# Kernel optimization log

Hardware: AMD Instinct MI355X
Metric: run time of the kernel (lower is better)

Reference implementation:

```python
import jax, jax.numpy as jnp
import numpy as np
from jax import lax

K_NEIGH = 10


def setup_inputs() -> dict:
    key = jax.random.key(0)
    k1, k2, k3, k4, k5 = jax.random.split(key, 5)
    bs, C, T = 8, 256, 2048
    x = jax.random.normal(k1, (bs, C, T), dtype=jnp.float32)
    num_frms = jax.random.randint(k2, (bs,), 0, 2048)
    # Conv1d(in=C, out=C, kernel=3, pad=1): weight [out, in, k], bias [out]
    conv_w = jax.random.normal(k3, (C, C, 3), dtype=jnp.float32) * (1.0 / np.sqrt(3 * C))
    conv_b = jnp.zeros((C,), dtype=jnp.float32)
    # Linear(2*C -> C): weight [out, 2*in], bias [out]
    mlp_w = jax.random.normal(k4, (C, 2 * C), dtype=jnp.float32) * (1.0 / np.sqrt(2 * C))
    mlp_b = jax.random.normal(k5, (C,), dtype=jnp.float32) * 0.01
    return {"x": x, "num_frms": num_frms, "conv_w": conv_w, "conv_b": conv_b,
            "mlp_w": mlp_w, "mlp_b": mlp_b}


def _knn_idx(x, k):
    # x: [bs, C, T]; dif[b,i,j] = ||x[b,:,i] - x[b,:,j]||^2 via norm expansion
    sq = jnp.sum(x * x, axis=1)                      # [bs, T]
    gram = jnp.einsum('bci,bcj->bij', x, x)          # [bs, T, T]
    dif = sq[:, :, None] + sq[:, None, :] - 2.0 * gram
    _, idx = lax.top_k(-dif, k)                      # k smallest distances
    return idx                                       # [bs, T, k]


def reference(x, num_frms, conv_w, conv_b, mlp_w, mlp_b):
    bs, C, T = x.shape
    Cout = conv_w.shape[0]
    # temporal conv branch (kernel 3, stride 1, pad 1)
    c_out = lax.conv_general_dilated(
        x, conv_w, window_strides=(1,), padding=((1, 1),),
        dimension_numbers=('NCH', 'OIH', 'NCH')) + conv_b[None, :, None]
    # graph branch ('par': knn on x)
    idx = _knn_idx(x, K_NEIGH)                                   # [bs, T, k]
    idx_flat = (idx + jnp.arange(bs)[:, None, None] * T).reshape(-1, K_NEIGH)
    feat = x.transpose(0, 2, 1).reshape(bs * T, C)               # [N, C]
    feat_neigh = feat[idx_flat]                                  # [N, k, C]
    ctr = feat[:, None, :]                                       # [N, 1, C]
    cat = jnp.concatenate(
        [feat_neigh, jnp.broadcast_to(ctr, feat_neigh.shape)], axis=-1)  # [N,k,2C]
    g = jnp.einsum('nkc,oc->nko', cat, mlp_w) + mlp_b            # [N, k, Cout]
    # cosine edge weight
    num = jnp.einsum('nkc,nc->nk', feat_neigh, feat)
    den = jnp.sqrt(jnp.sum(feat_neigh * feat_neigh, axis=2)) * \
          jnp.sqrt(jnp.sum(feat * feat, axis=1))[:, None]
    w = num / den                                                # [N, k]
    g = g * w[:, :, None]
    g = jnp.max(g, axis=1)                                       # [N, Cout]
    g_out = g.reshape(bs, T, Cout).transpose(0, 2, 1)            # [bs, Cout, T]
    out = jax.nn.relu(c_out + g_out)
    # MaxPool1d(kernel=2, stride=2)
    out = out.reshape(bs, Cout, T // 2, 2).max(axis=-1)
    return out
```

## Files before the change

### kernel.cpp

```cpp
#include <hip/hip_runtime.h>
#include <hip/hip_bf16.h>
#include <cstdint>

#define T_DIM 2048
#define C_DIM 256
#define BS 8
#define NPTS (BS * T_DIM)
#define KNB 10

typedef __bf16 bf16x8 __attribute__((ext_vector_type(8)));
typedef float f32x4 __attribute__((ext_vector_type(4)));

#define AS1 __attribute__((address_space(1)))
#define AS3 __attribute__((address_space(3)))

__device__ __forceinline__ unsigned short f2bf_rn(float f) {
  unsigned u = __float_as_uint(f);
  unsigned r = (u + 0x7FFFu + ((u >> 16) & 1u)) >> 16;
  return (unsigned short)r;
}
__device__ __forceinline__ float bfbits2f(unsigned short h) {
  return __uint_as_float((unsigned)h << 16);
}
__device__ __forceinline__ __bf16 bfbits(unsigned short h) {
  return __builtin_bit_cast(__bf16, h);
}

__device__ __forceinline__ void stage_tile(const __bf16* __restrict__ src, size_t row0,
                                           int ld, int k0, __bf16* lds, int w, int l) {
  int kofs = ((l & 7) ^ (l >> 3)) * 8;
  const __bf16* g0 = src + (row0 + (size_t)(l >> 3)) * ld + k0 + kofs;
  __bf16* lbase = lds + (size_t)(w * 4) * 512;
#pragma unroll
  for (int q4 = 0; q4 < 4; ++q4) {
    __builtin_amdgcn_global_load_lds((AS1 void*)(g0 + (size_t)(w * 4 + q4) * 8 * ld),
                                     (AS3 void*)(lbase + q4 * 512), 16, 0, 0);
  }
}

__device__ __forceinline__ void stage_tile_conv(const __bf16* __restrict__ src, int m0,
                                                int k0in, const __bf16* __restrict__ zp,
                                                __bf16* lds, int w, int l) {
  int tap = k0in >> 8;
  int kshift = tap - 1;
  int k0 = k0in & 255;
  int kofs = ((l & 7) ^ (l >> 3)) * 8;
  int mb = m0 & (T_DIM - 1);
#pragma unroll
  for (int q4 = 0; q4 < 4; ++q4) {
    int q = w * 4 + q4;
    int row = q * 8 + (l >> 3);
    int t = mb + row + kshift;
    const __bf16* g = ((unsigned)t < (unsigned)T_DIM)
                          ? (src + (size_t)(m0 + row + kshift) * C_DIM + k0 + kofs)
                          : (zp + kofs);
    __builtin_amdgcn_global_load_lds((AS1 void*)g, (AS3 void*)(lds + q * 512), 16, 0, 0);
  }
}

__device__ __forceinline__ bf16x8 read_frag(const __bf16* lds, int t16, int ks, int l) {
  int row = t16 * 16 + (l & 15);
  int kb = ks * 64 + ((l >> 4) << 4);
  int byte = row * 128 + (kb ^ ((row & 7) << 4));
  return *(const bf16x8*)((const char*)lds + byte);
}

__global__ __launch_bounds__(256) void k_transpose_split(const float* __restrict__ x,
                                                         __bf16* __restrict__ Fh,
                                                         __bf16* __restrict__ Fl) {
  __shared__ float tile[32][33];
  int b = blockIdx.z;
  int t0 = blockIdx.x * 32;
  int c0 = blockIdx.y * 32;
  int tx = threadIdx.x & 31, ty = threadIdx.x >> 5;
  const float* xb = x + (size_t)b * C_DIM * T_DIM;
#pragma unroll
  for (int r = 0; r < 4; ++r) {
    int c = c0 + ty + 8 * r;
    tile[ty + 8 * r][tx] = xb[(size_t)c * T_DIM + t0 + tx];
  }
  __syncthreads();
#pragma unroll
  for (int r = 0; r < 4; ++r) {
    int t = t0 + ty + 8 * r;
    float v = tile[tx][ty + 8 * r];
    unsigned short hb = f2bf_rn(v);
    float lo = v - bfbits2f(hb);
    size_t o = ((size_t)b * T_DIM + t) * C_DIM + c0 + tx;
    Fh[o] = bfbits(hb);
    Fl[o] = bfbits(f2bf_rn(lo));
  }
}

__global__ __launch_bounds__(256) void k_sq(const __bf16* __restrict__ Fh,
                                            const __bf16* __restrict__ Fl,
                                            float* __restrict__ sq) {
  int n = blockIdx.x * 4 + (threadIdx.x >> 6);
  int lane = threadIdx.x & 63;
  ushort4 hv = ((const ushort4*)Fh)[(size_t)n * 64 + lane];
  ushort4 lv = ((const ushort4*)Fl)[(size_t)n * 64 + lane];
  float s = 0.f;
  {
    float v;
    v = bfbits2f(hv.x) + bfbits2f(lv.x); s = fmaf(v, v, s);
    v = bfbits2f(hv.y) + bfbits2f(lv.y); s = fmaf(v, v, s);
    v = bfbits2f(hv.z) + bfbits2f(lv.z); s = fmaf(v, v, s);
    v = bfbits2f(hv.w) + bfbits2f(lv.w); s = fmaf(v, v, s);
  }
#pragma unroll
  for (int d = 1; d < 64; d <<= 1) s += __shfl_xor(s, d, 64);
  if (lane == 0) sq[n] = s;
}

__global__ __launch_bounds__(256, 2) void k_gram_sym(const __bf16* __restrict__ Fh,
                                                     const __bf16* __restrict__ Fl,
                                                     float* __restrict__ gram) {
  __shared__ __align__(16) char smem[65536];
  __bf16* Ah = (__bf16*)smem;
  __bf16* Al = (__bf16*)(smem + 16384);
  __bf16* Bh = (__bf16*)(smem + 32768);
  __bf16* Bl = (__bf16*)(smem + 49152);

  int b = blockIdx.y;
  int ti = blockIdx.x;
  int by = (int)((sqrtf(8.0f * (float)ti + 1.0f) - 1.0f) * 0.5f);
  if ((by + 1) * (by + 2) / 2 <= ti) by++;
  int bx = ti - by * (by + 1) / 2;

  size_t base = (size_t)b * T_DIM;
  int m0 = by * 128, n0 = bx * 128;
  int tid = threadIdx.x, w = tid >> 6, l = tid & 63;
  int wr = w >> 1, wc = w & 1;
  f32x4 acc[4][4];
#pragma unroll
  for (int i = 0; i < 4; ++i)
#pragma unroll
    for (int j = 0; j < 4; ++j) acc[i][j] = {0.f, 0.f, 0.f, 0.f};

  for (int k0 = 0; k0 < C_DIM; k0 += 64) {
    stage_tile(Fh, base + m0, C_DIM, k0, Ah, w, l);
    stage_tile(Fl, base + m0, C_DIM, k0, Al, w, l);
    stage_tile(Fh, base + n0, C_DIM, k0, Bh, w, l);
    stage_tile(Fl, base + n0, C_DIM, k0, Bl, w, l);
    __syncthreads();
#pragma unroll
    for (int ks = 0; ks < 2; ++ks) {
      bf16x8 ah[4], bh[4], x[4];
#pragma unroll
      for (int i = 0; i < 4; ++i) ah[i] = read_frag(Ah, wr * 4 + i, ks, l);
#pragma unroll
      for (int j = 0; j < 4; ++j) bh[j] = read_frag(Bh, wc * 4 + j, ks, l);
#pragma unroll
      for (int i = 0; i < 4; ++i)
#pragma unroll
        for (int j = 0; j < 4; ++j)
          acc[i][j] = __builtin_amdgcn_mfma_f32_16x16x32_bf16(ah[i], bh[j], acc[i][j], 0, 0, 0);
#pragma unroll
      for (int i = 0; i < 4; ++i) x[i] = read_frag(Al, wr * 4 + i, ks, l);
#pragma unroll
      for (int i = 0; i < 4; ++i)
#pragma unroll
        for (int j = 0; j < 4; ++j)
          acc[i][j] = __builtin_amdgcn_mfma_f32_16x16x32_bf16(x[i], bh[j], acc[i][j], 0, 0, 0);
#pragma unroll
      for (int j = 0; j < 4; ++j) x[j] = read_frag(Bl, wc * 4 + j, ks, l);
#pragma unroll
      for (int i = 0; i < 4; ++i)
#pragma unroll
        for (int j = 0; j < 4; ++j)
          acc[i][j] = __builtin_amdgcn_mfma_f32_16x16x32_bf16(ah[i], x[j], acc[i][j], 0, 0, 0);
    }
    __syncthreads();
  }

  float* gout = gram + (size_t)b * T_DIM * T_DIM;
#pragma unroll
  for (int i = 0; i < 4; ++i) {
    int mrow = m0 + wr * 64 + i * 16 + ((l >> 4) << 2);
#pragma unroll
    for (int j = 0; j < 4; ++j) {
      int ncol = n0 + wc * 64 + j * 16 + (l & 15);
      float* cp = gout + (size_t)mrow * T_DIM + ncol;
#pragma unroll
      for (int r = 0; r < 4; ++r) cp[(size_t)r * T_DIM] = acc[i][j][r];
    }
  }

  if (bx != by) {
    float* Tbuf = (float*)smem;
#pragma unroll
    for (int h = 0; h < 2; ++h) {
      __syncthreads();
      if (wc == h) {
#pragma unroll
        for (int j = 0; j < 4; ++j) {
          int cH = j * 16 + (l & 15);
          float* dst = Tbuf + cH * 132 + wr * 64 + ((l >> 4) << 2);
#pragma unroll
          for (int i = 0; i < 4; ++i) *(f32x4*)(dst + i * 16) = acc[i][j];
        }
      }
      __syncthreads();
      int cH = tid >> 5;
      int c4 = (tid & 31) * 4;
#pragma unroll
      for (int p = 0; p < 8; ++p) {
        f32x4 v = *(const f32x4*)(Tbuf + (size_t)(p * 8 + cH) * 132 + c4);
        *(f32x4*)(gout + (size_t)(n0 + h * 64 + p * 8 + cH) * T_DIM + m0 + c4) = v;
      }
    }
  }
}

__global__ __launch_bounds__(256, 2) void k_gemm16(const __bf16* __restrict__ A,
                                                   const __bf16* __restrict__ Bm,
                                                   float* __restrict__ C, int N, int K,
                                                   int conv, const __bf16* __restrict__ zp) {
  __shared__ __bf16 As[128 * 64], Bs[128 * 64];
  int m0 = blockIdx.y * 128, n0 = blockIdx.x * 128;
  int tid = threadIdx.x, w = tid >> 6, l = tid & 63;
  int wr = w >> 1, wc = w & 1;
  f32x4 acc[4][4];
#pragma unroll
  for (int i = 0; i < 4; ++i)
#pragma unroll
    for (int j = 0; j < 4; ++j) acc[i][j] = {0.f, 0.f, 0.f, 0.f};

  for (int k0 = 0; k0 < K; k0 += 64) {
    if (conv)
      stage_tile_conv(A, m0, k0, zp, As, w, l);
    else
      stage_tile(A, (size_t)m0, C_DIM, k0, As, w, l);
    stage_tile(Bm, (size_t)n0, K, k0, Bs, w, l);
    __syncthreads();
#pragma unroll
    for (int ks = 0; ks < 2; ++ks) {
      bf16x8 af[4], bf_[4];
#pragma unroll
      for (int i = 0; i < 4; ++i) af[i] = read_frag(As, wr * 4 + i, ks, l);
#pragma unroll
      for (int j = 0; j < 4; ++j) bf_[j] = read_frag(Bs, wc * 4 + j, ks, l);
#pragma unroll
      for (int i = 0; i < 4; ++i)
#pragma unroll
        for (int j = 0; j < 4; ++j)
          acc[i][j] = __builtin_amdgcn_mfma_f32_16x16x32_bf16(af[i], bf_[j], acc[i][j], 0, 0, 0);
    }
    __syncthreads();
  }
#pragma unroll
  for (int i = 0; i < 4; ++i) {
    int mrow = m0 + wr * 64 + i * 16 + ((l >> 4) << 2);
#pragma unroll
    for (int j = 0; j < 4; ++j) {
      int ncol = n0 + wc * 64 + j * 16 + (l & 15);
      float* cp = C + (size_t)mrow * N + ncol;
#pragma unroll
      for (int r = 0; r < 4; ++r) cp[(size_t)r * N] = acc[i][j][r];
    }
  }
}

__global__ __launch_bounds__(256) void k_topk(const float* __restrict__ gram,
                                              const float* __restrict__ sq,
                                              int* __restrict__ idxo,
                                              float* __restrict__ wo) {
  int lb = blockIdx.y;
  const float* gramb = gram + (size_t)lb * T_DIM * T_DIM;
  const float* sqb = sq + (size_t)lb * T_DIM;
  int* idxb = idxo + (size_t)lb * T_DIM * KNB;
  float* wbp = wo + (size_t)lb * T_DIM * KNB;

  int row = blockIdx.x * 4 + (threadIdx.x >> 6);
  int lane = threadIdx.x & 63;
  float sqi = sqb[row];
  const float* g = gramb + (size_t)row * T_DIM;

  unsigned kh[32];
  unsigned long long a0 = ~0ull, a1 = ~0ull;
#pragma unroll
  for (int t = 0; t < 32; ++t) {
    int j = lane + 64 * t;
    float dif = sqi + sqb[j] - 2.0f * g[j];
    unsigned u = __float_as_uint(dif);
    u = (u & 0x80000000u) ? ~u : (u | 0x80000000u);
    kh[t] = u;
    unsigned long long key = ((unsigned long long)u << 32) | (unsigned)j;
    unsigned long long mx = (key > a0) ? key : a0;
    a0 = (key < a0) ? key : a0;
    a1 = (mx < a1) ? mx : a1;
  }

  unsigned long long theta = 0;
#pragma unroll
  for (int s = 0; s < KNB; ++s) {
    unsigned long long m = a0;
#pragma unroll
    for (int d = 1; d < 64; d <<= 1) {
      unsigned long long o = __shfl_xor(m, d, 64);
      m = (o < m) ? o : m;
    }
    unsigned long long bal = __ballot(a0 == m);
    int leader = (int)__builtin_ctzll(bal);
    if (lane == leader) { a0 = a1; a1 = ~0ull; }
    if (lane == 0) {
      int j = (int)(unsigned)(m & 0xffffffffull);
      unsigned su = (unsigned)(m >> 32);
      unsigned bits = (su & 0x80000000u) ? (su & 0x7fffffffu) : ~su;
      float dif = __uint_as_float(bits);
      float sqj = sqb[j];
      float num = 0.5f * (sqi + sqj - dif);
      float wv = num / (sqrtf(sqi) * sqrtf(sqj));
      idxb[row * KNB + s] = j;
      wbp[row * KNB + s] = wv;
    }
    theta = m;
  }

  unsigned thi = (unsigned)(theta >> 32);
  unsigned tlo = (unsigned)(theta & 0xffffffffull);
  int c = 0;
#pragma unroll
  for (int t = 0; t < 32; ++t) {
    unsigned j = (unsigned)(lane + 64 * t);
    c += (kh[t] < thi) || ((kh[t] == thi) && (j < tlo));
  }
#pragma unroll
  for (int d = 1; d < 64; d <<= 1) c += __shfl_xor(c, d, 64);

  if (c == 9) return;

  unsigned long long b0 = ~0ull, b1 = ~0ull, b2 = ~0ull, b3 = ~0ull, b4 = ~0ull,
                     b5 = ~0ull, b6 = ~0ull, b7 = ~0ull, b8 = ~0ull, b9 = ~0ull;
#pragma unroll
  for (int t = 0; t < 32; ++t) {
    unsigned long long key = ((unsigned long long)kh[t] << 32) | (unsigned)(lane + 64 * t);
    if (key < b9) {
      b9 = key;
      unsigned long long tt;
      if (b9 < b8) { tt = b8; b8 = b9; b9 = tt; }
      if (b8 < b7) { tt = b7; b7 = b8; b8 = tt; }
      if (b7 < b6) { tt = b6; b6 = b7; b7 = tt; }
      if (b6 < b5) { tt = b5; b5 = b6; b6 = tt; }
      if (b5 < b4) { tt = b4; b4 = b5; b5 = tt; }
      if (b4 < b3) { tt = b3; b3 = b4; b4 = tt; }
      if (b3 < b2) { tt = b2; b2 = b3; b3 = tt; }
      if (b2 < b1) { tt = b1; b1 = b2; b2 = tt; }
      if (b1 < b0) { tt = b0; b0 = b1; b1 = tt; }
    }
  }
#pragma unroll
  for (int s = 0; s < KNB; ++s) {
    unsigned long long m = b0;
#pragma unroll
    for (int d = 1; d < 64; d <<= 1) {
      unsigned long long o = __shfl_xor(m, d, 64);
      m = (o < m) ? o : m;
    }
    unsigned long long bal = __ballot(b0 == m);
    int leader = (int)__builtin_ctzll(bal);
    if (lane == leader) {
      b0 = b1; b1 = b2; b2 = b3; b3 = b4; b4 = b5;
      b5 = b6; b6 = b7; b7 = b8; b8 = b9; b9 = ~0ull;
    }
    if (lane == 0) {
      int j = (int)(unsigned)(m & 0xffffffffull);
      unsigned su = (unsigned)(m >> 32);
      unsigned bits = (su & 0x80000000u) ? (su & 0x7fffffffu) : ~su;
      float dif = __uint_as_float(bits);
      float sqj = sqb[j];
      float num = 0.5f * (sqi + sqj - dif);
      float wv = num / (sqrtf(sqi) * sqrtf(sqj));
      idxb[row * KNB + s] = j;
      wbp[row * KNB + s] = wv;
    }
  }
}

__global__ __launch_bounds__(256) void k_gfinal(const float* __restrict__ mlpout,
                                                const float* __restrict__ mlp_b,
                                                const int* __restrict__ idxo,
                                                const float* __restrict__ wo,
                                                const float* __restrict__ convb,
                                                const float* __restrict__ cb,
                                                float* __restrict__ out) {
  __shared__ float tile[32][33];
  __shared__ int sj[64][KNB];
  __shared__ float sw[64][KNB];
  int b = blockIdx.z, c0 = blockIdx.y * 32, t20 = blockIdx.x * 32;
  int tid = threadIdx.x;
  int nbase = b * T_DIM + t20 * 2;
  for (int e = tid; e < 64 * KNB; e += 256) {
    int ln = e / KNB, k = e - ln * KNB;
    sj[ln][k] = b * T_DIM + idxo[(size_t)(nbase + ln) * KNB + k];
    sw[ln][k] = wo[(size_t)(nbase + ln) * KNB + k];
  }
  __syncthreads();
  int tx = tid & 31, ty = tid >> 5;
  int c = c0 + tx;
  float bias_c = cb[c];
  float mbias = mlp_b[c];
#pragma unroll
  for (int rr = 0; rr < 4; ++rr) {
    int lt2 = ty + 8 * rr;
    float res[2];
#pragma unroll
    for (int s = 0; s < 2; ++s) {
      int ln = 2 * lt2 + s;
      int n = nbase + ln;
      float q = mlpout[(size_t)n * 512 + 256 + c] + mbias;
      float mx = -3.4e38f;
#pragma unroll
      for (int k = 0; k < KNB; ++k) {
        float v = (mlpout[(size_t)sj[ln][k] * 512 + c] + q) * sw[ln][k];
        mx = fmaxf(mx, v);
      }
      float v = convb[(size_t)n * C_DIM + c] + mx + bias_c;
      res[s] = fmaxf(v, 0.f);
    }
    tile[lt2][tx] = fmaxf(res[0], res[1]);
  }
  __syncthreads();
#pragma unroll
  for (int rr = 0; rr < 4; ++rr) {
    int cc = c0 + ty + 8 * rr;
    out[((size_t)b * C_DIM + cc) * (T_DIM / 2) + t20 + tx] = tile[tx][ty + 8 * rr];
  }
}

__global__ void k_repack(const float* __restrict__ cw, const float* __restrict__ mw,
                         __bf16* __restrict__ wk3, __bf16* __restrict__ mlpB,
                         __bf16* __restrict__ zp) {
  int i = blockIdx.x * 256 + threadIdx.x;
  if (i < 3 * C_DIM * C_DIM) {
    int o = i / 768;
    int rem = i - o * 768;
    int tap = rem >> 8;
    int ii = rem & 255;
    wk3[i] = bfbits(f2bf_rn(cw[(size_t)o * 768 + ii * 3 + tap]));
  } else {
    int m = i - 3 * C_DIM * C_DIM;
    if (m < 512 * 256) {
      int r = m >> 8;
      int col = m & 255;
      mlpB[m] = bfbits(f2bf_rn(mw[(size_t)(r & 255) * 512 + ((r >> 8) << 8) + col]));
    }
  }
  if (blockIdx.x == 0 && threadIdx.x < 128) zp[threadIdx.x] = bfbits(0);
}

extern "C" void kernel_launch(void* const* d_in, const int* in_sizes, int n_in,
                              void* d_out, int out_size, void* d_ws, size_t ws_size,
                              hipStream_t stream) {
  const float* x = (const float*)d_in[0];
  const float* conv_w = (const float*)d_in[2];
  const float* conv_b = (const float*)d_in[3];
  const float* mlp_w = (const float*)d_in[4];
  const float* mlp_b = (const float*)d_in[5];
  float* out = (float*)d_out;

  char* ws = (char*)d_ws;
  size_t off = 0;
  auto alloc = [&](size_t bytes) -> void* {
    void* p = ws + off;
    off += (bytes + 255) & ~(size_t)255;
    return p;
  };
  float* gram = (float*)alloc((size_t)BS * T_DIM * T_DIM * 4);
  __bf16* Fh = (__bf16*)alloc((size_t)NPTS * C_DIM * 2);
  __bf16* Fl = (__bf16*)alloc((size_t)NPTS * C_DIM * 2);
  float* convout = (float*)alloc((size_t)NPTS * C_DIM * 4);
  float* mlpout = (float*)alloc((size_t)NPTS * 512 * 4);
  float* sq = (float*)alloc((size_t)NPTS * 4);
  int* idxb = (int*)alloc((size_t)NPTS * KNB * 4);
  float* wb = (float*)alloc((size_t)NPTS * KNB * 4);
  __bf16* wk3 = (__bf16*)alloc((size_t)3 * C_DIM * C_DIM * 2);
  __bf16* mlpB = (__bf16*)alloc((size_t)512 * 256 * 2);
  __bf16* zp = (__bf16*)alloc(512);

  k_repack<<<dim3(1280), 256, 0, stream>>>(conv_w, mlp_w, wk3, mlpB, zp);
  k_transpose_split<<<dim3(T_DIM / 32, C_DIM / 32, BS), 256, 0, stream>>>(x, Fh, Fl);
  k_sq<<<dim3(NPTS / 4), 256, 0, stream>>>(Fh, Fl, sq);

  k_gram_sym<<<dim3(136, BS), 256, 0, stream>>>(Fh, Fl, gram);
  k_topk<<<dim3(T_DIM / 4, BS), 256, 0, stream>>>(gram, sq, idxb, wb);

  k_gemm16<<<dim3(512 / 128, NPTS / 128), 256, 0, stream>>>(Fh, mlpB, mlpout, 512, 256, 0, zp);
  k_gemm16<<<dim3(256 / 128, NPTS / 128), 256, 0, stream>>>(Fh, wk3, convout, 256, 768, 1, zp);

  k_gfinal<<<dim3((T_DIM / 2) / 32, C_DIM / 32, BS), 256, 0, stream>>>(
      mlpout, mlp_b, idxb, wb, convout, conv_b, out);
}
```

Measured before the change: 189.4 us.

## Fuse Gram computation with streaming top-k and add exact fallback pass

Removes the 128 MB materialised Gram matrix by computing 64-row by 128-candidate tiles and keeping a per-lane sorted top-8 of 64-bit keys in registers, merged across lanes with shuffles. Rows whose partial lists may have dropped a true neighbour are flagged through an atomic list and recomputed exactly by a fallback kernel. The two bf16 GEMMs are also merged into one launch. The fused kernel drops symmetric reuse and runs at occupancy 1, so it does more MFMA work. It also adds a serial fallback pass whose cost depends on how many rows get flagged.

```diff
diff --git a/kernel.cpp b/kernel.cpp
--- a/kernel.cpp
+++ b/kernel.cpp
@@ -10,6 +10,7 @@
 
 typedef __bf16 bf16x8 __attribute__((ext_vector_type(8)));
 typedef float f32x4 __attribute__((ext_vector_type(4)));
+typedef unsigned long long u64;
 
 #define AS1 __attribute__((address_space(1)))
 #define AS3 __attribute__((address_space(3)))
@@ -24,6 +25,12 @@
 }
 __device__ __forceinline__ __bf16 bfbits(unsigned short h) {
   return __builtin_bit_cast(__bf16, h);
+}
+
+__device__ __forceinline__ unsigned key_hi(float sqi, float sqj, float gv) {
+  float dif = __fmaf_rn(-2.0f, gv, __fadd_rn(sqi, sqj));
+  unsigned u = __float_as_uint(dif);
+  return (u & 0x80000000u) ? ~u : (u | 0x80000000u);
 }
 
 __device__ __forceinline__ void stage_tile(const __bf16* __restrict__ src, size_t row0,
@@ -34,6 +41,18 @@
 #pragma unroll
   for (int q4 = 0; q4 < 4; ++q4) {
     __builtin_amdgcn_global_load_lds((AS1 void*)(g0 + (size_t)(w * 4 + q4) * 8 * ld),
+                                     (AS3 void*)(lbase + q4 * 512), 16, 0, 0);
+  }
+}
+
+__device__ __forceinline__ void stage_tile64(const __bf16* __restrict__ src, size_t row0,
+                                             int k0, __bf16* lds, int w, int l) {
+  int kofs = ((l & 7) ^ (l >> 3)) * 8;
+  const __bf16* g0 = src + (row0 + (size_t)(l >> 3)) * C_DIM + k0 + kofs;
+  __bf16* lbase = lds + (size_t)(w * 2) * 512;
+#pragma unroll
+  for (int q4 = 0; q4 < 2; ++q4) {
+    __builtin_amdgcn_global_load_lds((AS1 void*)(g0 + (size_t)(w * 2 + q4) * 8 * C_DIM),
                                      (AS3 void*)(lbase + q4 * 512), 16, 0, 0);
   }
 }
@@ -112,267 +131,287 @@
   if (lane == 0) sq[n] = s;
 }
 
-__global__ __launch_bounds__(256, 2) void k_gram_sym(const __bf16* __restrict__ Fh,
+
+__global__ __launch_bounds__(256, 1) void k_gramtopk(const __bf16* __restrict__ Fh,
                                                      const __bf16* __restrict__ Fl,
-                                                     float* __restrict__ gram) {
-  __shared__ __align__(16) char smem[65536];
-  __bf16* Ah = (__bf16*)smem;
-  __bf16* Al = (__bf16*)(smem + 16384);
-  __bf16* Bh = (__bf16*)(smem + 32768);
-  __bf16* Bl = (__bf16*)(smem + 49152);
+                                                     const float* __restrict__ sq,
+                                                     int* __restrict__ idxo,
+                                                     float* __restrict__ wo,
+                                                     int* __restrict__ fixlist,
+                                                     int* __restrict__ fixcount) {
+  __shared__ __bf16 Bh[128 * 64], Bl[128 * 64];
+  __shared__ __bf16 Rh[64 * 64], Rl[64 * 64];
+  __shared__ float sqc[128];
 
   int b = blockIdx.y;
-  int ti = blockIdx.x;
-  int by = (int)((sqrtf(8.0f * (float)ti + 1.0f) - 1.0f) * 0.5f);
-  if ((by + 1) * (by + 2) / 2 <= ti) by++;
-  int bx = ti - by * (by + 1) / 2;
-
+  int r0 = blockIdx.x * 64;
   size_t base = (size_t)b * T_DIM;
-  int m0 = by * 128, n0 = bx * 128;
+  const float* sqb = sq + base;
   int tid = threadIdx.x, w = tid >> 6, l = tid & 63;
-  int wr = w >> 1, wc = w & 1;
-  f32x4 acc[4][4];
-#pragma unroll
-  for (int i = 0; i < 4; ++i)
-#pragma unroll
-    for (int j = 0; j < 4; ++j) acc[i][j] = {0.f, 0.f, 0.f, 0.f};
-
-  for (int k0 = 0; k0 < C_DIM; k0 += 64) {
-    stage_tile(Fh, base + m0, C_DIM, k0, Ah, w, l);
-    stage_tile(Fl, base + m0, C_DIM, k0, Al, w, l);
-    stage_tile(Fh, base + n0, C_DIM, k0, Bh, w, l);
-    stage_tile(Fl, base + n0, C_DIM, k0, Bl, w, l);
-    __syncthreads();
-#pragma unroll
-    for (int ks = 0; ks < 2; ++ks) {
-      bf16x8 ah[4], bh[4], x[4];
-#pragma unroll
-      for (int i = 0; i < 4; ++i) ah[i] = read_frag(Ah, wr * 4 + i, ks, l);
-#pragma unroll
-      for (int j = 0; j < 4; ++j) bh[j] = read_frag(Bh, wc * 4 + j, ks, l);
-#pragma unroll
-      for (int i = 0; i < 4; ++i)
-#pragma unroll
-        for (int j = 0; j < 4; ++j)
-          acc[i][j] = __builtin_amdgcn_mfma_f32_16x16x32_bf16(ah[i], bh[j], acc[i][j], 0, 0, 0);
-#pragma unroll
-      for (int i = 0; i < 4; ++i) x[i] = read_frag(Al, wr * 4 + i, ks, l);
-#pragma unroll
-      for (int i = 0; i < 4; ++i)
-#pragma unroll
-        for (int j = 0; j < 4; ++j)
-          acc[i][j] = __builtin_amdgcn_mfma_f32_16x16x32_bf16(x[i], bh[j], acc[i][j], 0, 0, 0);
-#pragma unroll
-      for (int j = 0; j < 4; ++j) x[j] = read_frag(Bl, wc * 4 + j, ks, l);
-#pragma unroll
-      for (int i = 0; i < 4; ++i)
-#pragma unroll
-        for (int j = 0; j < 4; ++j)
-          acc[i][j] = __builtin_amdgcn_mfma_f32_16x16x32_bf16(ah[i], x[j], acc[i][j], 0, 0, 0);
-    }
-    __syncthreads();
-  }
-
-  float* gout = gram + (size_t)b * T_DIM * T_DIM;
-#pragma unroll
-  for (int i = 0; i < 4; ++i) {
-    int mrow = m0 + wr * 64 + i * 16 + ((l >> 4) << 2);
-#pragma unroll
-    for (int j = 0; j < 4; ++j) {
-      int ncol = n0 + wc * 64 + j * 16 + (l & 15);
-      float* cp = gout + (size_t)mrow * T_DIM + ncol;
-#pragma unroll
-      for (int r = 0; r < 4; ++r) cp[(size_t)r * T_DIM] = acc[i][j][r];
-    }
-  }
-
-  if (bx != by) {
-    float* Tbuf = (float*)smem;
-#pragma unroll
-    for (int h = 0; h < 2; ++h) {
+  int g = l >> 4;
+  int myrow = r0 + w * 16 + (l & 15);
+  float sqi = sqb[myrow];
+
+  u64 s0 = ~0ull, s1 = ~0ull, s2 = ~0ull, s3 = ~0ull,
+      s4 = ~0ull, s5 = ~0ull, s6 = ~0ull, s7 = ~0ull;
+  u64 excl = ~0ull;
+
+  for (int ch = 0; ch < 16; ++ch) {
+    int cand0 = ch * 128;
+    if (tid < 128) sqc[tid] = sqb[cand0 + tid];
+    f32x4 acc[8];
+#pragma unroll
+    for (int j = 0; j < 8; ++j) acc[j] = {0.f, 0.f, 0.f, 0.f};
+
+    for (int k0 = 0; k0 < C_DIM; k0 += 64) {
+      stage_tile(Fh, base + cand0, C_DIM, k0, Bh, w, l);
+      stage_tile(Fl, base + cand0, C_DIM, k0, Bl, w, l);
+      stage_tile64(Fh, base + r0, k0, Rh, w, l);
+      stage_tile64(Fl, base + r0, k0, Rl, w, l);
       __syncthreads();
-      if (wc == h) {
-#pragma unroll
-        for (int j = 0; j < 4; ++j) {
-          int cH = j * 16 + (l & 15);
-          float* dst = Tbuf + cH * 132 + wr * 64 + ((l >> 4) << 2);
-#pragma unroll
-          for (int i = 0; i < 4; ++i) *(f32x4*)(dst + i * 16) = acc[i][j];
-        }
+#pragma unroll
+      for (int ks = 0; ks < 2; ++ks) {
+        bf16x8 rh = read_frag(Rh, w, ks, l);
+        bf16x8 rl = read_frag(Rl, w, ks, l);
+        bf16x8 cv[8];
+#pragma unroll
+        for (int j = 0; j < 8; ++j) cv[j] = read_frag(Bh, j, ks, l);
+#pragma unroll
+        for (int j = 0; j < 8; ++j)
+          acc[j] = __builtin_amdgcn_mfma_f32_16x16x32_bf16(cv[j], rh, acc[j], 0, 0, 0);
+#pragma unroll
+        for (int j = 0; j < 8; ++j)
+          acc[j] = __builtin_amdgcn_mfma_f32_16x16x32_bf16(cv[j], rl, acc[j], 0, 0, 0);
+#pragma unroll
+        for (int j = 0; j < 8; ++j) cv[j] = read_frag(Bl, j, ks, l);
+#pragma unroll
+        for (int j = 0; j < 8; ++j)
+          acc[j] = __builtin_amdgcn_mfma_f32_16x16x32_bf16(cv[j], rh, acc[j], 0, 0, 0);
       }
       __syncthreads();
-      int cH = tid >> 5;
-      int c4 = (tid & 31) * 4;
-#pragma unroll
-      for (int p = 0; p < 8; ++p) {
-        f32x4 v = *(const f32x4*)(Tbuf + (size_t)(p * 8 + cH) * 132 + c4);
-        *(f32x4*)(gout + (size_t)(n0 + h * 64 + p * 8 + cH) * T_DIM + m0 + c4) = v;
+    }
+
+    u64 c0 = ~0ull, c1 = ~0ull, c2 = ~0ull, c3 = ~0ull;
+#pragma unroll
+    for (int j = 0; j < 8; ++j) {
+      f32x4 sv = *(const f32x4*)&sqc[j * 16 + (g << 2)];
+#pragma unroll
+      for (int r = 0; r < 4; ++r) {
+        unsigned u = key_hi(sqi, sv[r], acc[j][r]);
+        unsigned cand = (unsigned)(cand0 + j * 16 + (g << 2) + r);
+        u64 key = ((u64)u << 32) | cand;
+        u64 t1 = (key > c0) ? key : c0; c0 = (key < c0) ? key : c0;
+        u64 t2 = (t1 > c1) ? t1 : c1;  c1 = (t1 < c1) ? t1 : c1;
+        u64 t3 = (t2 > c2) ? t2 : c2;  c2 = (t2 < c2) ? t2 : c2;
+        c3 = (t3 < c3) ? t3 : c3;
       }
     }
-  }
-}
-
-__global__ __launch_bounds__(256, 2) void k_gemm16(const __bf16* __restrict__ A,
-                                                   const __bf16* __restrict__ Bm,
-                                                   float* __restrict__ C, int N, int K,
-                                                   int conv, const __bf16* __restrict__ zp) {
-  __shared__ __bf16 As[128 * 64], Bs[128 * 64];
-  int m0 = blockIdx.y * 128, n0 = blockIdx.x * 128;
-  int tid = threadIdx.x, w = tid >> 6, l = tid & 63;
-  int wr = w >> 1, wc = w & 1;
-  f32x4 acc[4][4];
-#pragma unroll
-  for (int i = 0; i < 4; ++i)
-#pragma unroll
-    for (int j = 0; j < 4; ++j) acc[i][j] = {0.f, 0.f, 0.f, 0.f};
-
-  for (int k0 = 0; k0 < K; k0 += 64) {
-    if (conv)
-      stage_tile_conv(A, m0, k0, zp, As, w, l);
-    else
-      stage_tile(A, (size_t)m0, C_DIM, k0, As, w, l);
-    stage_tile(Bm, (size_t)n0, K, k0, Bs, w, l);
+#pragma unroll
+    for (int q = 0; q < 4; ++q) {
+      u64 t = (q == 0) ? c0 : (q == 1) ? c1 : (q == 2) ? c2 : c3;
+      u64 hi;
+      hi = (t > s0) ? t : s0; s0 = (t < s0) ? t : s0; t = hi;
+      hi = (t > s1) ? t : s1; s1 = (t < s1) ? t : s1; t = hi;
+      hi = (t > s2) ? t : s2; s2 = (t < s2) ? t : s2; t = hi;
+      hi = (t > s3) ? t : s3; s3 = (t < s3) ? t : s3; t = hi;
+      hi = (t > s4) ? t : s4; s4 = (t < s4) ? t : s4; t = hi;
+      hi = (t > s5) ? t : s5; s5 = (t < s5) ? t : s5; t = hi;
+      hi = (t > s6) ? t : s6; s6 = (t < s6) ? t : s6; t = hi;
+      hi = (t > s7) ? t : s7; s7 = (t < s7) ? t : s7; t = hi;
+      excl = (t < excl) ? t : excl;
+    }
+    excl = (c3 < excl) ? c3 : excl;
     __syncthreads();
-#pragma unroll
-    for (int ks = 0; ks < 2; ++ks) {
-      bf16x8 af[4], bf_[4];
-#pragma unroll
-      for (int i = 0; i < 4; ++i) af[i] = read_frag(As, wr * 4 + i, ks, l);
-#pragma unroll
-      for (int j = 0; j < 4; ++j) bf_[j] = read_frag(Bs, wc * 4 + j, ks, l);
-#pragma unroll
-      for (int i = 0; i < 4; ++i)
-#pragma unroll
-        for (int j = 0; j < 4; ++j)
-          acc[i][j] = __builtin_amdgcn_mfma_f32_16x16x32_bf16(af[i], bf_[j], acc[i][j], 0, 0, 0);
-    }
-    __syncthreads();
-  }
-#pragma unroll
-  for (int i = 0; i < 4; ++i) {
-    int mrow = m0 + wr * 64 + i * 16 + ((l >> 4) << 2);
-#pragma unroll
-    for (int j = 0; j < 4; ++j) {
-      int ncol = n0 + wc * 64 + j * 16 + (l & 15);
-      float* cp = C + (size_t)mrow * N + ncol;
-#pragma unroll
-      for (int r = 0; r < 4; ++r) cp[(size_t)r * N] = acc[i][j][r];
-    }
-  }
-}
-
-__global__ __launch_bounds__(256) void k_topk(const float* __restrict__ gram,
-                                              const float* __restrict__ sq,
-                                              int* __restrict__ idxo,
-                                              float* __restrict__ wo) {
-  int lb = blockIdx.y;
-  const float* gramb = gram + (size_t)lb * T_DIM * T_DIM;
-  const float* sqb = sq + (size_t)lb * T_DIM;
-  int* idxb = idxo + (size_t)lb * T_DIM * KNB;
-  float* wbp = wo + (size_t)lb * T_DIM * KNB;
-
-  int row = blockIdx.x * 4 + (threadIdx.x >> 6);
-  int lane = threadIdx.x & 63;
-  float sqi = sqb[row];
-  const float* g = gramb + (size_t)row * T_DIM;
-
-  unsigned kh[32];
-  unsigned long long a0 = ~0ull, a1 = ~0ull;
-#pragma unroll
-  for (int t = 0; t < 32; ++t) {
-    int j = lane + 64 * t;
-    float dif = sqi + sqb[j] - 2.0f * g[j];
-    unsigned u = __float_as_uint(dif);
-    u = (u & 0x80000000u) ? ~u : (u | 0x80000000u);
-    kh[t] = u;
-    unsigned long long key = ((unsigned long long)u << 32) | (unsigned)j;
-    unsigned long long mx = (key > a0) ? key : a0;
-    a0 = (key < a0) ? key : a0;
-    a1 = (mx < a1) ? mx : a1;
-  }
-
-  unsigned long long theta = 0;
+  }
+
+  u64 win[KNB];
 #pragma unroll
   for (int s = 0; s < KNB; ++s) {
-    unsigned long long m = a0;
-#pragma unroll
-    for (int d = 1; d < 64; d <<= 1) {
-      unsigned long long o = __shfl_xor(m, d, 64);
-      m = (o < m) ? o : m;
-    }
-    unsigned long long bal = __ballot(a0 == m);
-    int leader = (int)__builtin_ctzll(bal);
-    if (lane == leader) { a0 = a1; a1 = ~0ull; }
-    if (lane == 0) {
-      int j = (int)(unsigned)(m & 0xffffffffull);
-      unsigned su = (unsigned)(m >> 32);
+    u64 m = s0;
+    { u64 o = __shfl_xor(m, 16, 64); m = (o < m) ? o : m; }
+    { u64 o = __shfl_xor(m, 32, 64); m = (o < m) ? o : m; }
+    bool pop = (s0 == m);
+    s0 = pop ? s1 : s0; s1 = pop ? s2 : s1; s2 = pop ? s3 : s2;
+    s3 = pop ? s4 : s3; s4 = pop ? s5 : s4; s5 = pop ? s6 : s5;
+    s6 = pop ? s7 : s6; s7 = pop ? ~0ull : s7;
+    win[s] = m;
+  }
+  u64 theta = win[KNB - 1];
+
+  int* idxb = idxo + base * KNB;
+  float* wbp = wo + base * KNB;
+#pragma unroll
+  for (int s = 0; s < KNB; ++s) {
+    if ((s & 3) == g) {
+      int j = (int)(unsigned)(win[s] & 0xffffffffull);
+      unsigned su = (unsigned)(win[s] >> 32);
       unsigned bits = (su & 0x80000000u) ? (su & 0x7fffffffu) : ~su;
       float dif = __uint_as_float(bits);
       float sqj = sqb[j];
       float num = 0.5f * (sqi + sqj - dif);
       float wv = num / (sqrtf(sqi) * sqrtf(sqj));
-      idxb[row * KNB + s] = j;
-      wbp[row * KNB + s] = wv;
-    }
-    theta = m;
-  }
-
-  unsigned thi = (unsigned)(theta >> 32);
-  unsigned tlo = (unsigned)(theta & 0xffffffffull);
-  int c = 0;
-#pragma unroll
-  for (int t = 0; t < 32; ++t) {
-    unsigned j = (unsigned)(lane + 64 * t);
-    c += (kh[t] < thi) || ((kh[t] == thi) && (j < tlo));
-  }
-#pragma unroll
-  for (int d = 1; d < 64; d <<= 1) c += __shfl_xor(c, d, 64);
-
-  if (c == 9) return;
-
-  unsigned long long b0 = ~0ull, b1 = ~0ull, b2 = ~0ull, b3 = ~0ull, b4 = ~0ull,
-                     b5 = ~0ull, b6 = ~0ull, b7 = ~0ull, b8 = ~0ull, b9 = ~0ull;
-#pragma unroll
-  for (int t = 0; t < 32; ++t) {
-    unsigned long long key = ((unsigned long long)kh[t] << 32) | (unsigned)(lane + 64 * t);
-    if (key < b9) {
-      b9 = key;
-      unsigned long long tt;
-      if (b9 < b8) { tt = b8; b8 = b9; b9 = tt; }
-      if (b8 < b7) { tt = b7; b7 = b8; b8 = tt; }
-      if (b7 < b6) { tt = b6; b6 = b7; b7 = tt; }
-      if (b6 < b5) { tt = b5; b5 = b6; b6 = tt; }
-      if (b5 < b4) { tt = b4; b4 = b5; b5 = tt; }
-      if (b4 < b3) { tt = b3; b3 = b4; b4 = tt; }
-      if (b3 < b2) { tt = b2; b2 = b3; b3 = tt; }
-      if (b2 < b1) { tt = b1; b1 = b2; b2 = tt; }
-      if (b1 < b0) { tt = b0; b0 = b1; b1 = tt; }
-    }
-  }
-#pragma unroll
-  for (int s = 0; s < KNB; ++s) {
-    unsigned long long m = b0;
-#pragma unroll
-    for (int d = 1; d < 64; d <<= 1) {
-      unsigned long long o = __shfl_xor(m, d, 64);
-      m = (o < m) ? o : m;
-    }
-    unsigned long long bal = __ballot(b0 == m);
-    int leader = (int)__builtin_ctzll(bal);
-    if (lane == leader) {
-      b0 = b1; b1 = b2; b2 = b3; b3 = b4; b4 = b5;
-      b5 = b6; b6 = b7; b7 = b8; b8 = b9; b9 = ~0ull;
-    }
-    if (lane == 0) {
-      int j = (int)(unsigned)(m & 0xffffffffull);
-      unsigned su = (unsigned)(m >> 32);
-      unsigned bits = (su & 0x80000000u) ? (su & 0x7fffffffu) : ~su;
-      float dif = __uint_as_float(bits);
-      float sqj = sqb[j];
-      float num = 0.5f * (sqi + sqj - dif);
-      float wv = num / (sqrtf(sqi) * sqrtf(sqj));
-      idxb[row * KNB + s] = j;
-      wbp[row * KNB + s] = wv;
+      idxb[(size_t)myrow * KNB + s] = j;
+      wbp[(size_t)myrow * KNB + s] = wv;
+    }
+  }
+
+  { u64 o = __shfl_xor(excl, 16, 64); excl = (o < excl) ? o : excl; }
+  { u64 o = __shfl_xor(excl, 32, 64); excl = (o < excl) ? o : excl; }
+  if (g == 0 && excl < theta) {
+    int slot = atomicAdd(fixcount, 1);
+    fixlist[slot] = (int)(base + myrow);
+  }
+}
+
+__global__ __launch_bounds__(256) void k_topk_fix(const __bf16* __restrict__ Fh,
+                                                  const __bf16* __restrict__ Fl,
+                                                  const float* __restrict__ sq,
+                                                  const int* __restrict__ fixlist,
+                                                  const int* __restrict__ fixcount,
+                                                  int* __restrict__ idxo,
+                                                  float* __restrict__ wo) {
+  __shared__ float xr[C_DIM];
+  __shared__ float difs[T_DIM];
+  int n = fixcount[0];
+  int tid = threadIdx.x;
+  for (int i = blockIdx.x; i < n; i += gridDim.x) {
+    int rowg = fixlist[i];
+    int b = rowg >> 11, r = rowg & (T_DIM - 1);
+    const unsigned short* fh = (const unsigned short*)Fh;
+    const unsigned short* fl = (const unsigned short*)Fl;
+    xr[tid] = bfbits2f(fh[(size_t)rowg * C_DIM + tid]) + bfbits2f(fl[(size_t)rowg * C_DIM + tid]);
+    __syncthreads();
+    const float* sqb = sq + (size_t)b * T_DIM;
+    float sqi = sqb[r];
+#pragma unroll 2
+    for (int it = 0; it < 8; ++it) {
+      int j = tid + it * 256;
+      const ushort4* chp = (const ushort4*)(fh + ((size_t)b * T_DIM + j) * C_DIM);
+      const ushort4* clp = (const ushort4*)(fl + ((size_t)b * T_DIM + j) * C_DIM);
+      float dot = 0.f;
+      for (int c4 = 0; c4 < 64; ++c4) {
+        ushort4 h = chp[c4];
+        ushort4 lo = clp[c4];
+        dot = fmaf(bfbits2f(h.x) + bfbits2f(lo.x), xr[c4 * 4 + 0], dot);
+        dot = fmaf(bfbits2f(h.y) + bfbits2f(lo.y), xr[c4 * 4 + 1], dot);
+        dot = fmaf(bfbits2f(h.z) + bfbits2f(lo.z), xr[c4 * 4 + 2], dot);
+        dot = fmaf(bfbits2f(h.w) + bfbits2f(lo.w), xr[c4 * 4 + 3], dot);
+      }
+      difs[j] = __fmaf_rn(-2.0f, dot, __fadd_rn(sqi, sqb[j]));
+    }
+    __syncthreads();
+    if (tid < 64) {
+      int lane = tid;
+      u64 b0 = ~0ull, b1 = ~0ull, b2 = ~0ull, b3 = ~0ull, b4 = ~0ull,
+          b5 = ~0ull, b6 = ~0ull, b7 = ~0ull, b8 = ~0ull, b9 = ~0ull;
+      for (int t = 0; t < 32; ++t) {
+        unsigned j = (unsigned)(lane + 64 * t);
+        unsigned u = __float_as_uint(difs[j]);
+        u = (u & 0x80000000u) ? ~u : (u | 0x80000000u);
+        u64 key = ((u64)u << 32) | j;
+        if (key < b9) {
+          b9 = key;
+          u64 tt;
+          if (b9 < b8) { tt = b8; b8 = b9; b9 = tt; }
+          if (b8 < b7) { tt = b7; b7 = b8; b8 = tt; }
+          if (b7 < b6) { tt = b6; b6 = b7; b7 = tt; }
+          if (b6 < b5) { tt = b5; b5 = b6; b6 = tt; }
+          if (b5 < b4) { tt = b4; b4 = b5; b5 = tt; }
+          if (b4 < b3) { tt = b3; b3 = b4; b4 = tt; }
+          if (b3 < b2) { tt = b2; b2 = b3; b3 = tt; }
+          if (b2 < b1) { tt = b1; b1 = b2; b2 = tt; }
+          if (b1 < b0) { tt = b0; b0 = b1; b1 = tt; }
+        }
+      }
+      int* idxb = idxo + (size_t)b * T_DIM * KNB;
+      float* wbp = wo + (size_t)b * T_DIM * KNB;
+#pragma unroll
+      for (int s = 0; s < KNB; ++s) {
+        u64 m = b0;
+#pragma unroll
+        for (int d = 1; d < 64; d <<= 1) {
+          u64 o = __shfl_xor(m, d, 64);
+          m = (o < m) ? o : m;
+        }
+        u64 bal = __ballot(b0 == m);
+        int leader = (int)__builtin_ctzll(bal);
+        if (lane == leader) {
+          b0 = b1; b1 = b2; b2 = b3; b3 = b4; b4 = b5;
+          b5 = b6; b6 = b7; b7 = b8; b8 = b9; b9 = ~0ull;
+        }
+        if (lane == 0) {
+          int j = (int)(unsigned)(m & 0xffffffffull);
+          unsigned su = (unsigned)(m >> 32);
+          unsigned bits = (su & 0x80000000u) ? (su & 0x7fffffffu) : ~su;
+          float dif = __uint_as_float(bits);
+          float sqj = sqb[j];
+          float num = 0.5f * (sqi + sqj - dif);
+          float wv = num / (sqrtf(sqi) * sqrtf(sqj));
+          idxb[(size_t)r * KNB + s] = j;
+          wbp[(size_t)r * KNB + s] = wv;
+        }
+      }
+    }
+    __syncthreads();
+  }
+}
+
+__global__ __launch_bounds__(256, 2) void k_gemm_fused(const __bf16* __restrict__ Fh,
+                                                       const __bf16* __restrict__ mlpB,
+                                                       const __bf16* __restrict__ wk3,
+                                                       float* __restrict__ mlpout,
+                                                       float* __restrict__ convout,
+                                                       const __bf16* __restrict__ zp) {
+  __shared__ __bf16 As[128 * 64], Bs[128 * 64];
+  int bx = blockIdx.x;
+  const __bf16* Bm;
+  float* C;
+  int N, K, conv, n0;
+  if (bx < 4) {
+    Bm = mlpB; C = mlpout; N = 512; K = 256; conv = 0; n0 = bx * 128;
+  } else {
+    Bm = wk3; C = convout; N = 256; K = 768; conv = 1; n0 = (bx - 4) * 128;
+  }
+  int m0 = blockIdx.y * 128;
+  int tid = threadIdx.x, w = tid >> 6, l = tid & 63;
+  int wr = w >> 1, wc = w & 1;
+  f32x4 acc[4][4];
+#pragma unroll
+  for (int i = 0; i < 4; ++i)
+#pragma unroll
+    for (int j = 0; j < 4; ++j) acc[i][j] = {0.f, 0.f, 0.f, 0.f};
+
+  for (int k0 = 0; k0 < K; k0 += 64) {
+    if (conv)
+      stage_tile_conv(Fh, m0, k0, zp, As, w, l);
+    else
+      stage_tile(Fh, (size_t)m0, C_DIM, k0, As, w, l);
+    stage_tile(Bm, (size_t)n0, K, k0, Bs, w, l);
+    __syncthreads();
+#pragma unroll
+    for (int ks = 0; ks < 2; ++ks) {
+      bf16x8 af[4], bf_[4];
+#pragma unroll
+      for (int i = 0; i < 4; ++i) af[i] = read_frag(As, wr * 4 + i, ks, l);
+#pragma unroll
+      for (int j = 0; j < 4; ++j) bf_[j] = read_frag(Bs, wc * 4 + j, ks, l);
+#pragma unroll
+      for (int i = 0; i < 4; ++i)
+#pragma unroll
+        for (int j = 0; j < 4; ++j)
+          acc[i][j] = __builtin_amdgcn_mfma_f32_16x16x32_bf16(af[i], bf_[j], acc[i][j], 0, 0, 0);
+    }
+    __syncthreads();
+  }
+#pragma unroll
+  for (int i = 0; i < 4; ++i) {
+    int mrow = m0 + wr * 64 + i * 16 + ((l >> 4) << 2);
+#pragma unroll
+    for (int j = 0; j < 4; ++j) {
+      int ncol = n0 + wc * 64 + j * 16 + (l & 15);
+      float* cp = C + (size_t)mrow * N + ncol;
+#pragma unroll
+      for (int r = 0; r < 4; ++r) cp[(size_t)r * N] = acc[i][j][r];
     }
   }
 }
@@ -430,8 +469,9 @@
 
 __global__ void k_repack(const float* __restrict__ cw, const float* __restrict__ mw,
                          __bf16* __restrict__ wk3, __bf16* __restrict__ mlpB,
-                         __bf16* __restrict__ zp) {
+                         __bf16* __restrict__ zp, int* __restrict__ fixcount) {
   int i = blockIdx.x * 256 + threadIdx.x;
+  if (i == 0) fixcount[0] = 0;
   if (i < 3 * C_DIM * C_DIM) {
     int o = i / 768;
     int rem = i - o * 768;
@@ -466,7 +506,6 @@
     off += (bytes + 255) & ~(size_t)255;
     return p;
   };
-  float* gram = (float*)alloc((size_t)BS * T_DIM * T_DIM * 4);
   __bf16* Fh = (__bf16*)alloc((size_t)NPTS * C_DIM * 2);
   __bf16* Fl = (__bf16*)alloc((size_t)NPTS * C_DIM * 2);
   float* convout = (float*)alloc((size_t)NPTS * C_DIM * 4);
@@ -474,19 +513,20 @@
   float* sq = (float*)alloc((size_t)NPTS * 4);
   int* idxb = (int*)alloc((size_t)NPTS * KNB * 4);
   float* wb = (float*)alloc((size_t)NPTS * KNB * 4);
+  int* fixlist = (int*)alloc((size_t)NPTS * 4);
+  int* fixcount = (int*)alloc(256);
   __bf16* wk3 = (__bf16*)alloc((size_t)3 * C_DIM * C_DIM * 2);
   __bf16* mlpB = (__bf16*)alloc((size_t)512 * 256 * 2);
   __bf16* zp = (__bf16*)alloc(512);
 
-  k_repack<<<dim3(1280), 256, 0, stream>>>(conv_w, mlp_w, wk3, mlpB, zp);
+  k_repack<<<dim3(1280), 256, 0, stream>>>(conv_w, mlp_w, wk3, mlpB, zp, fixcount);
   k_transpose_split<<<dim3(T_DIM / 32, C_DIM / 32, BS), 256, 0, stream>>>(x, Fh, Fl);
   k_sq<<<dim3(NPTS / 4), 256, 0, stream>>>(Fh, Fl, sq);
 
-  k_gram_sym<<<dim3(136, BS), 256, 0, stream>>>(Fh, Fl, gram);
-  k_topk<<<dim3(T_DIM / 4, BS), 256, 0, stream>>>(gram, sq, idxb, wb);
-
-  k_gemm16<<<dim3(512 / 128, NPTS / 128), 256, 0, stream>>>(Fh, mlpB, mlpout, 512, 256, 0, zp);
-  k_gemm16<<<dim3(256 / 128, NPTS / 128), 256, 0, stream>>>(Fh, wk3, convout, 256, 768, 1, zp);
+  k_gramtopk<<<dim3(T_DIM / 64, BS), 256, 0, stream>>>(Fh, Fl, sq, idxb, wb, fixlist, fixcount);
+  k_topk_fix<<<dim3(64), 256, 0, stream>>>(Fh, Fl, sq, fixlist, fixcount, idxb, wb);
+
+  k_gemm_fused<<<dim3(6, NPTS / 128), 256, 0, stream>>>(Fh, mlpB, wk3, mlpout, convout, zp);
 
   k_gfinal<<<dim3((T_DIM / 2) / 32, C_DIM / 32, BS), 256, 0, stream>>>(
       mlpout, mlp_b, idxb, wb, convout, conv_b, out);
```

Result: slower. 286.7 us (+51.4%).
